# Kernel optimization log

Measured on AMD Instinct MI355X. Metric: run time of the kernel, lower is better.

The kernel has to match this reference:

```python
import jax, jax.numpy as jnp
import numpy as np

LN_EPS = 1e-5

def _layernorm(x, gamma, beta):
    mu = jnp.mean(x, axis=-1, keepdims=True)
    var = jnp.var(x, axis=-1, keepdims=True)
    return (x - mu) * jax.lax.rsqrt(var + LN_EPS) * gamma + beta

def setup_inputs() -> dict:
    key = jax.random.key(0)
    ks = jax.random.split(key, 4)
    B, s, d, L = 8, 192, 512, 8
    h = 2048  # embed_dim * 2
    return {
        "lags": jax.random.normal(ks[0], (B, s, d, L), dtype=jnp.float32),
        "gamma1": jnp.ones((d,), jnp.float32),
        "beta1": jnp.zeros((d,), jnp.float32),
        "W1": jax.random.normal(ks[1], (d, h), jnp.float32) * (1.0 / np.sqrt(d)),
        "b1": jnp.zeros((h,), jnp.float32),
        "W2": jax.random.normal(ks[2], (h, d), jnp.float32) * (1.0 / np.sqrt(h)),
        "b2": jnp.zeros((d,), jnp.float32),
        "gamma3": jnp.ones((d,), jnp.float32),
        "beta3": jnp.zeros((d,), jnp.float32),
    }

def reference(lags, gamma1, beta1, W1, b1, W2, b2, gamma3, beta3):
    B, s, d, L = lags.shape
    # (B, s, d, L) -> (B, s, L, d) -> (B, S=s*L, d)
    x = jnp.transpose(lags, (0, 1, 3, 2)).reshape(B, s * L, d)
    scale = 1.0 / jnp.sqrt(jnp.asarray(d, x.dtype))
    # single-head, unprojected attention: scores = X X^T / sqrt(d)
    scores = jnp.einsum('bqd,bkd->bqk', x, x) * scale  # [B, S, S]
    attn = jax.nn.softmax(scores, axis=-1)
    attn_out = jnp.einsum('bqk,bkd->bqd', attn, x)
    q = _layernorm(x + attn_out, gamma1, beta1)
    ff = jnp.dot(jax.nn.gelu(jnp.dot(q, W1) + b1, approximate=False), W2) + b2
    out = _layernorm(q + ff, gamma3, beta3)
    # (B, S, d) -> (B, s, L, d) -> (B, s, d, L)
    return jnp.transpose(out.reshape(B, s, L, d), (0, 1, 3, 2))
```

## Files before the change

kernel.cpp:

```cpp
#include <hip/hip_runtime.h>
#include <hip/hip_bf16.h>
#include <math.h>

#define B_ 8
#define S_ 192
#define D_ 512
#define L_ 8
#define SQ 1536
#define H_ 2048
#define NROW (B_*SQ)
#define SCALE_QK 0.04419417382415922f

typedef unsigned short ushort_t;
typedef unsigned int uint_t;
typedef __attribute__((ext_vector_type(8))) short bf16x8;
typedef __attribute__((ext_vector_type(4))) float f32x4;

__device__ __forceinline__ float bfu2f(ushort_t u) { return __uint_as_float((unsigned)u << 16); }
__device__ __forceinline__ ushort_t f2bfu(float f) {
  __hip_bfloat16 h = __float2bfloat16(f);
  return *reinterpret_cast<ushort_t*>(&h);
}

__device__ __forceinline__ float gelu_fast(float x) {
  float z = fabsf(x) * 0.70710678118654752f;
  float t = __builtin_amdgcn_rcpf(fmaf(0.3275911f, z, 1.0f));
  float p = fmaf(1.061405429f, t, -1.453152027f);
  p = fmaf(p, t, 1.421413741f);
  p = fmaf(p, t, -0.284496736f);
  p = fmaf(p, t, 0.254829592f);
  p = p * t;
  float e = __expf(-z * z);
  float erfz = fmaf(-p, e, 1.0f);
  float s = (x >= 0.0f) ? erfz : -erfz;
  return 0.5f * x * (1.0f + s);
}

__device__ __forceinline__ void gl_lds16(const ushort_t* g, ushort_t* l) {
  __builtin_amdgcn_global_load_lds(
      (const __attribute__((address_space(1))) unsigned int*)g,
      (__attribute__((address_space(3))) unsigned int*)l, 16, 0, 0);
}

__global__ __launch_bounds__(256) void k_build_x_f(const float* __restrict__ lags,
                                                   float* __restrict__ x,
                                                   ushort_t* __restrict__ x_bf) {
  __shared__ float tile[512][9];
  const int tid = threadIdx.x;
  const float* in = lags + (size_t)blockIdx.x * 4096;
  #pragma unroll
  for (int it = 0; it < 4; ++it) {
    int f = (tid + it * 256) * 4;
    float4 v = *reinterpret_cast<const float4*>(in + f);
    int k = f >> 3, l0 = f & 7;
    tile[k][l0] = v.x; tile[k][l0 + 1] = v.y; tile[k][l0 + 2] = v.z; tile[k][l0 + 3] = v.w;
  }
  __syncthreads();
  const int l = tid >> 5, kbase = tid & 31;
  const size_t r = (size_t)blockIdx.x * 8 + l;
  #pragma unroll
  for (int j = 0; j < 16; ++j) {
    int k = kbase + 32 * j;
    float v = tile[k][l];
    x[r * D_ + k] = v;
    x_bf[r * D_ + k] = f2bfu(v);
  }
}

__global__ __launch_bounds__(256) void k_xt(const ushort_t* __restrict__ x_bf,
                                            ushort_t* __restrict__ xT) {
  __shared__ ushort_t tile[64][65];
  int t0 = blockIdx.x * 64, d0 = blockIdx.y * 64;
  const ushort_t* X = x_bf + (size_t)blockIdx.z * SQ * D_;
  ushort_t* XT = xT + (size_t)blockIdx.z * SQ * D_;
  for (int i = threadIdx.x; i < 4096; i += 256) {
    int tt = i >> 6, dd = i & 63;
    tile[dd][tt] = X[(size_t)(t0 + tt) * D_ + d0 + dd];
  }
  __syncthreads();
  for (int i = threadIdx.x; i < 4096; i += 256) {
    int dd = i >> 6, tt = i & 63;
    XT[(size_t)(d0 + dd) * SQ + t0 + tt] = tile[dd][tt];
  }
}

__global__ __launch_bounds__(256) void k_wt(const float* __restrict__ W,
                                            ushort_t* __restrict__ Wt,
                                            int K, int N) {
  __shared__ ushort_t tile[64][65];
  int n0 = blockIdx.x * 64, k0 = blockIdx.y * 64;
  for (int i = threadIdx.x; i < 4096; i += 256) {
    int kk = i >> 6, nn = i & 63;
    tile[nn][kk] = f2bfu(W[(size_t)(k0 + kk) * N + n0 + nn]);
  }
  __syncthreads();
  for (int i = threadIdx.x; i < 4096; i += 256) {
    int nn = i >> 6, kk = i & 63;
    Wt[(size_t)(n0 + nn) * K + k0 + kk] = tile[nn][kk];
  }
}

template<int MODE>
__global__ __launch_bounds__(256) void k_gemm(const ushort_t* __restrict__ A,
                                              const ushort_t* __restrict__ Bt,
                                              const float* __restrict__ bias,
                                              void* __restrict__ Cout,
                                              int M, int K, int N,
                                              size_t sAz, size_t sBz, size_t sCz,
                                              float scale) {
  A  += (size_t)blockIdx.z * sAz;
  Bt += (size_t)blockIdx.z * sBz;
  __shared__ ushort_t As[128 * 64];
  __shared__ ushort_t Bs[128 * 64];
  const int tid = threadIdx.x;
  const int m0 = blockIdx.y * 128, n0 = blockIdx.x * 128;
  const int w = tid >> 6, lane = tid & 63;
  const int wr = w >> 1, wc = w & 1;
  const int l15 = lane & 15, quad = lane >> 4;
  const int lrow8 = lane >> 3;
  const int cg = ((lane & 7) ^ lrow8) * 8;
  const int xsw = l15 & 7;
  ushort_t* lA = &As[(w * 32) * 64];
  ushort_t* lB = &Bs[(w * 32) * 64];

  f32x4 acc[4][4];
  if (MODE <= 1) {
    #pragma unroll
    for (int nj = 0; nj < 4; ++nj) {
      float bv = bias[n0 + wc * 64 + nj * 16 + l15];
      #pragma unroll
      for (int mi = 0; mi < 4; ++mi) acc[mi][nj] = (f32x4){bv, bv, bv, bv};
    }
  } else {
    #pragma unroll
    for (int nj = 0; nj < 4; ++nj)
      #pragma unroll
      for (int mi = 0; mi < 4; ++mi) acc[mi][nj] = (f32x4){0.f, 0.f, 0.f, 0.f};
  }

  for (int k0 = 0; k0 < K; k0 += 64) {
    const ushort_t* gA = A  + (size_t)(m0 + w * 32 + lrow8) * K + k0 + cg;
    const ushort_t* gB = Bt + (size_t)(n0 + w * 32 + lrow8) * K + k0 + cg;
    __syncthreads();
    #pragma unroll
    for (int j = 0; j < 4; ++j) {
      gl_lds16(gA + (size_t)(j * 8) * K, lA + j * 8 * 64);
      gl_lds16(gB + (size_t)(j * 8) * K, lB + j * 8 * 64);
    }
    __syncthreads();
    #pragma unroll
    for (int kk = 0; kk < 2; ++kk) {
      const int csel = ((kk * 4 + quad) ^ xsw) * 8;
      bf16x8 af[4], bfv[4];
      #pragma unroll
      for (int mi = 0; mi < 4; ++mi)
        af[mi] = *reinterpret_cast<const bf16x8*>(&As[(wr * 64 + mi * 16 + l15) * 64 + csel]);
      #pragma unroll
      for (int nj = 0; nj < 4; ++nj)
        bfv[nj] = *reinterpret_cast<const bf16x8*>(&Bs[(wc * 64 + nj * 16 + l15) * 64 + csel]);
      #pragma unroll
      for (int mi = 0; mi < 4; ++mi)
        #pragma unroll
        for (int nj = 0; nj < 4; ++nj)
          acc[mi][nj] = __builtin_amdgcn_mfma_f32_16x16x32_bf16(af[mi], bfv[nj], acc[mi][nj], 0, 0, 0);
    }
  }

  ushort_t* Cb = (ushort_t*)Cout + (size_t)blockIdx.z * sCz;
  float*    Cf = (float*)Cout    + (size_t)blockIdx.z * sCz;
  #pragma unroll
  for (int mi = 0; mi < 4; ++mi)
    #pragma unroll
    for (int nj = 0; nj < 4; ++nj) {
      int gc = n0 + wc * 64 + nj * 16 + l15;
      #pragma unroll
      for (int r = 0; r < 4; ++r) {
        int gr = m0 + wr * 64 + mi * 16 + quad * 4 + r;
        float v = acc[mi][nj][r];
        if (MODE == 0) {
          Cb[(size_t)gr * N + gc] = f2bfu(gelu_fast(v));
        } else if (MODE == 1) {
          Cf[(size_t)gr * N + gc] = v;
        } else if (MODE == 2) {
          Cb[(size_t)gr * N + gc] = f2bfu(v * scale);
        } else {
          Cf[(size_t)gr * N + gc] = v;
        }
      }
    }
}

__global__ __launch_bounds__(256) void k_softmax_bf(ushort_t* __restrict__ sc) {
  uint_t* row = (uint_t*)(sc + (size_t)blockIdx.z * SQ * SQ + (size_t)blockIdx.x * SQ);
  int tid = threadIdx.x;
  __shared__ float red[8];
  float v[6];
  float m = -1e30f;
  #pragma unroll
  for (int k = 0; k < 3; ++k) {
    uint_t u = row[tid + k * 256];
    v[2*k]   = __uint_as_float(u << 16);
    v[2*k+1] = __uint_as_float(u & 0xffff0000u);
    m = fmaxf(m, fmaxf(v[2*k], v[2*k+1]));
  }
  #pragma unroll
  for (int o = 32; o > 0; o >>= 1) m = fmaxf(m, __shfl_down(m, o));
  if ((tid & 63) == 0) red[tid >> 6] = m;
  __syncthreads();
  m = fmaxf(fmaxf(red[0], red[1]), fmaxf(red[2], red[3]));
  __syncthreads();
  float ssum = 0.f;
  #pragma unroll
  for (int k = 0; k < 6; ++k) { v[k] = expf(v[k] - m); ssum += v[k]; }
  #pragma unroll
  for (int o = 32; o > 0; o >>= 1) ssum += __shfl_down(ssum, o);
  if ((tid & 63) == 0) red[4 + (tid >> 6)] = ssum;
  __syncthreads();
  float inv = 1.0f / (red[4] + red[5] + red[6] + red[7]);
  #pragma unroll
  for (int k = 0; k < 3; ++k) {
    uint_t lo = f2bfu(v[2*k] * inv);
    uint_t hi = f2bfu(v[2*k+1] * inv);
    row[tid + k * 256] = (hi << 16) | lo;
  }
}

__global__ __launch_bounds__(256) void k_ln1b(const float* __restrict__ x,
                                              const float* __restrict__ attn,
                                              const float* __restrict__ g,
                                              const float* __restrict__ be,
                                              ushort_t* __restrict__ qbf) {
  size_t base = (size_t)blockIdx.x * D_;
  int tid = threadIdx.x;
  __shared__ float rl[8];
  float v0 = x[base + tid] + attn[base + tid];
  float v1 = x[base + tid + 256] + attn[base + tid + 256];
  float s = v0 + v1, sq = v0 * v0 + v1 * v1;
  #pragma unroll
  for (int o = 32; o > 0; o >>= 1) { s += __shfl_down(s, o); sq += __shfl_down(sq, o); }
  int lane = tid & 63, wid = tid >> 6;
  if (lane == 0) { rl[wid] = s; rl[4 + wid] = sq; }
  __syncthreads();
  s = rl[0] + rl[1] + rl[2] + rl[3];
  sq = rl[4] + rl[5] + rl[6] + rl[7];
  float mean = s * (1.0f / 512.0f);
  float var = sq * (1.0f / 512.0f) - mean * mean;
  float rstd = rsqrtf(var + 1e-5f);
  qbf[base + tid]       = f2bfu((v0 - mean) * rstd * g[tid] + be[tid]);
  qbf[base + tid + 256] = f2bfu((v1 - mean) * rstd * g[tid + 256] + be[tid + 256]);
}

__global__ __launch_bounds__(256) void k_ln3_f(const float* __restrict__ y,
                                               const ushort_t* __restrict__ qbf,
                                               const float* __restrict__ g3,
                                               const float* __restrict__ be3,
                                               float* __restrict__ out) {
  __shared__ float ynorm[8][512];
  const int tid = threadIdx.x;
  const int w = tid >> 6, lane = tid & 63;
  #pragma unroll
  for (int rr = 0; rr < 2; ++rr) {
    int l = 2 * w + rr;
    size_t t = (size_t)blockIdx.x * 8 + l;
    float v[8];
    float s = 0.f, sq = 0.f;
    #pragma unroll
    for (int j = 0; j < 8; ++j) {
      int k = lane + 64 * j;
      v[j] = y[t * D_ + k] + bfu2f(qbf[t * D_ + k]);
      s += v[j]; sq += v[j] * v[j];
    }
    #pragma unroll
    for (int o = 32; o > 0; o >>= 1) { s += __shfl_down(s, o); sq += __shfl_down(sq, o); }
    s = __shfl(s, 0); sq = __shfl(sq, 0);
    float mean = s * (1.0f / 512.0f);
    float var = sq * (1.0f / 512.0f) - mean * mean;
    float rstd = rsqrtf(var + 1e-5f);
    #pragma unroll
    for (int j = 0; j < 8; ++j) {
      int k = lane + 64 * j;
      ynorm[l][k] = (v[j] - mean) * rstd * g3[k] + be3[k];
    }
  }
  __syncthreads();
  float* ob = out + (size_t)blockIdx.x * 4096;
  #pragma unroll
  for (int kk = 0; kk < 2; ++kk) {
    int k = tid * 2 + kk;
    float4 lo = make_float4(ynorm[0][k], ynorm[1][k], ynorm[2][k], ynorm[3][k]);
    float4 hi = make_float4(ynorm[4][k], ynorm[5][k], ynorm[6][k], ynorm[7][k]);
    *reinterpret_cast<float4*>(ob + (size_t)k * 8)     = lo;
    *reinterpret_cast<float4*>(ob + (size_t)k * 8 + 4) = hi;
  }
}

#define TS 64
#define KT 16
__global__ __launch_bounds__(256) void k_build_x_s(const float* __restrict__ lags,
                                                   float* __restrict__ x, int b_base) {
  int idx = blockIdx.x * 256 + threadIdx.x;
  int k = idx & (D_ - 1);
  int r = idx >> 9;
  int b = b_base + r / SQ;
  int t = r - (r / SQ) * SQ;
  int si = t >> 3, l = t & 7;
  size_t src = (((size_t)(b * S_ + si) * D_ + k) << 3) + l;
  x[idx] = lags[src];
}

__global__ __launch_bounds__(256) void k_scores(const float* __restrict__ x,
                                                float* __restrict__ sc, int b_base) {
  const float* A = x;
  float* C = sc;
  __shared__ float As[TS][KT + 1];
  __shared__ float Bs[TS][KT + 1];
  int tx = threadIdx.x & 15, ty = threadIdx.x >> 4;
  int j0 = blockIdx.x * TS, i0 = blockIdx.y * TS;
  float acc[4][4] = {};
  int lk = threadIdx.x & 15, lr = threadIdx.x >> 4;
  for (int k0 = 0; k0 < D_; k0 += KT) {
    #pragma unroll
    for (int it = 0; it < 4; ++it) {
      As[lr + 16 * it][lk] = A[(size_t)(i0 + lr + 16 * it) * D_ + k0 + lk];
      Bs[lr + 16 * it][lk] = A[(size_t)(j0 + lr + 16 * it) * D_ + k0 + lk];
    }
    __syncthreads();
    #pragma unroll
    for (int kk = 0; kk < KT; ++kk) {
      float a[4], bb[4];
      #pragma unroll
      for (int r = 0; r < 4; ++r) a[r] = As[ty * 4 + r][kk];
      #pragma unroll
      for (int c = 0; c < 4; ++c) bb[c] = Bs[tx * 4 + c][kk];
      #pragma unroll
      for (int r = 0; r < 4; ++r)
        #pragma unroll
        for (int c = 0; c < 4; ++c) acc[r][c] = fmaf(a[r], bb[c], acc[r][c]);
    }
    __syncthreads();
  }
  #pragma unroll
  for (int r = 0; r < 4; ++r) {
    float4 v = make_float4(acc[r][0]*SCALE_QK, acc[r][1]*SCALE_QK,
                           acc[r][2]*SCALE_QK, acc[r][3]*SCALE_QK);
    *reinterpret_cast<float4*>(&C[(size_t)(i0 + ty*4 + r) * SQ + j0 + tx*4]) = v;
  }
}

__global__ __launch_bounds__(256) void k_softmax(float* __restrict__ sc) {
  float* row = sc + (size_t)blockIdx.x * SQ;
  int tid = threadIdx.x;
  __shared__ float red[8];
  float m = -1e30f;
  for (int j = tid; j < SQ; j += 256) m = fmaxf(m, row[j]);
  #pragma unroll
  for (int o = 32; o > 0; o >>= 1) m = fmaxf(m, __shfl_down(m, o));
  if ((tid & 63) == 0) red[tid >> 6] = m;
  __syncthreads();
  m = fmaxf(fmaxf(red[0], red[1]), fmaxf(red[2], red[3]));
  __syncthreads();
  float ssum = 0.f;
  for (int j = tid; j < SQ; j += 256) { float e = expf(row[j] - m); row[j] = e; ssum += e; }
  #pragma unroll
  for (int o = 32; o > 0; o >>= 1) ssum += __shfl_down(ssum, o);
  if ((tid & 63) == 0) red[4 + (tid >> 6)] = ssum;
  __syncthreads();
  float inv = 1.0f / (red[4] + red[5] + red[6] + red[7]);
  for (int j = tid; j < SQ; j += 256) row[j] *= inv;
}

__global__ __launch_bounds__(256) void k_attn(const float* __restrict__ x,
                                              const float* __restrict__ sc,
                                              float* __restrict__ attn) {
  const float* X = x;
  const float* P = sc;
  float* O = attn;
  __shared__ float Ps[TS][KT + 1];
  __shared__ float Xs[KT][TS];
  int tx = threadIdx.x & 15, ty = threadIdx.x >> 4;
  int j0 = blockIdx.x * TS, i0 = blockIdx.y * TS;
  float acc[4][4] = {};
  int lk = threadIdx.x & 15, lr = threadIdx.x >> 4;
  int lc = threadIdx.x & 63, lrow = threadIdx.x >> 6;
  for (int k0 = 0; k0 < SQ; k0 += KT) {
    #pragma unroll
    for (int it = 0; it < 4; ++it)
      Ps[lr + 16 * it][lk] = P[(size_t)(i0 + lr + 16 * it) * SQ + k0 + lk];
    #pragma unroll
    for (int it = 0; it < 4; ++it)
      Xs[lrow + 4 * it][lc] = X[(size_t)(k0 + lrow + 4 * it) * D_ + j0 + lc];
    __syncthreads();
    #pragma unroll
    for (int kk = 0; kk < KT; ++kk) {
      float a[4], bb[4];
      #pragma unroll
      for (int r = 0; r < 4; ++r) a[r] = Ps[ty * 4 + r][kk];
      #pragma unroll
      for (int c = 0; c < 4; ++c) bb[c] = Xs[kk][tx * 4 + c];
      #pragma unroll
      for (int r = 0; r < 4; ++r)
        #pragma unroll
        for (int c = 0; c < 4; ++c) acc[r][c] = fmaf(a[r], bb[c], acc[r][c]);
    }
    __syncthreads();
  }
  #pragma unroll
  for (int r = 0; r < 4; ++r) {
    float4 v = make_float4(acc[r][0], acc[r][1], acc[r][2], acc[r][3]);
    *reinterpret_cast<float4*>(&O[(size_t)(i0 + ty*4 + r) * D_ + j0 + tx*4]) = v;
  }
}

__global__ __launch_bounds__(256) void k_ln1(const float* __restrict__ x,
                                             const float* __restrict__ attn,
                                             const float* __restrict__ g,
                                             const float* __restrict__ be,
                                             float* __restrict__ qout) {
  size_t base = (size_t)blockIdx.x * D_;
  int tid = threadIdx.x;
  __shared__ float rl[8];
  float v0 = x[base + tid] + attn[base + tid];
  float v1 = x[base + tid + 256] + attn[base + tid + 256];
  float s = v0 + v1, sq = v0 * v0 + v1 * v1;
  #pragma unroll
  for (int o = 32; o > 0; o >>= 1) { s += __shfl_down(s, o); sq += __shfl_down(sq, o); }
  int lane = tid & 63, wid = tid >> 6;
  if (lane == 0) { rl[wid] = s; rl[4 + wid] = sq; }
  __syncthreads();
  s = rl[0] + rl[1] + rl[2] + rl[3];
  sq = rl[4] + rl[5] + rl[6] + rl[7];
  float mean = s * (1.0f / 512.0f);
  float var = sq * (1.0f / 512.0f) - mean * mean;
  float rstd = rsqrtf(var + 1e-5f);
  qout[base + tid]       = (v0 - mean) * rstd * g[tid] + be[tid];
  qout[base + tid + 256] = (v1 - mean) * rstd * g[tid + 256] + be[tid + 256];
}

__global__ __launch_bounds__(256, 2) void k_ffn(
    const float* __restrict__ q,
    const float* __restrict__ W1, const float* __restrict__ b1,
    const float* __restrict__ W2, const float* __restrict__ b2,
    const float* __restrict__ g3, const float* __restrict__ be3,
    float* __restrict__ out, int row_base)
{
  __shared__ float qs[8][D_];
  __shared__ float mid[8][H_];
  const int tid = threadIdx.x;
  const int row0 = blockIdx.x * 8;
  for (int idx = tid; idx < 8 * D_; idx += 256)
    qs[idx >> 9][idx & (D_ - 1)] = q[(size_t)row0 * D_ + idx];
  __syncthreads();
  float acc[8][8];
  {
    float4 bA = *reinterpret_cast<const float4*>(b1 + (tid << 3));
    float4 bB = *reinterpret_cast<const float4*>(b1 + (tid << 3) + 4);
    float bv[8] = {bA.x, bA.y, bA.z, bA.w, bB.x, bB.y, bB.z, bB.w};
    #pragma unroll
    for (int jj = 0; jj < 8; ++jj)
      #pragma unroll
      for (int r = 0; r < 8; ++r) acc[jj][r] = bv[jj];
  }
  for (int k4 = 0; k4 < D_ / 4; ++k4) {
    float4 qv[8];
    #pragma unroll
    for (int r = 0; r < 8; ++r)
      qv[r] = *reinterpret_cast<const float4*>(&qs[r][k4 << 2]);
    #pragma unroll
    for (int kk = 0; kk < 4; ++kk) {
      const int k = (k4 << 2) + kk;
      float4 wA = *reinterpret_cast<const float4*>(W1 + (size_t)k * H_ + (tid << 3));
      float4 wB = *reinterpret_cast<const float4*>(W1 + (size_t)k * H_ + (tid << 3) + 4);
      float wv[8] = {wA.x, wA.y, wA.z, wA.w, wB.x, wB.y, wB.z, wB.w};
      #pragma unroll
      for (int r = 0; r < 8; ++r) {
        float qk = (kk == 0) ? qv[r].x : (kk == 1) ? qv[r].y : (kk == 2) ? qv[r].z : qv[r].w;
        #pragma unroll
        for (int jj = 0; jj < 8; ++jj) acc[jj][r] = fmaf(qk, wv[jj], acc[jj][r]);
      }
    }
  }
  #pragma unroll
  for (int jj = 0; jj < 8; ++jj)
    #pragma unroll
    for (int r = 0; r < 8; ++r) {
      float v = acc[jj][r];
      mid[r][(tid << 3) + jj] = 0.5f * v * (1.0f + erff(v * 0.70710678118654752f));
    }
  __syncthreads();
  float acc2[8][2];
  {
    float b20 = b2[tid << 1], b21 = b2[(tid << 1) + 1];
    #pragma unroll
    for (int r = 0; r < 8; ++r) { acc2[r][0] = b20; acc2[r][1] = b21; }
  }
  for (int j4 = 0; j4 < H_ / 4; ++j4) {
    float4 mv[8];
    #pragma unroll
    for (int r = 0; r < 8; ++r)
      mv[r] = *reinterpret_cast<const float4*>(&mid[r][j4 << 2]);
    #pragma unroll
    for (int kk = 0; kk < 4; ++kk) {
      const int j = (j4 << 2) + kk;
      float2 wv = *reinterpret_cast<const float2*>(W2 + (size_t)j * D_ + (tid << 1));
      #pragma unroll
      for (int r = 0; r < 8; ++r) {
        float m = (kk == 0) ? mv[r].x : (kk == 1) ? mv[r].y : (kk == 2) ? mv[r].z : mv[r].w;
        acc2[r][0] = fmaf(m, wv.x, acc2[r][0]);
        acc2[r][1] = fmaf(m, wv.y, acc2[r][1]);
      }
    }
  }
  __syncthreads();
  float* ys = &mid[0][0];
  #pragma unroll
  for (int r = 0; r < 8; ++r) {
    ys[r * D_ + (tid << 1)]     = qs[r][(tid << 1)]     + acc2[r][0];
    ys[r * D_ + (tid << 1) + 1] = qs[r][(tid << 1) + 1] + acc2[r][1];
  }
  __syncthreads();
  float g3a = g3[tid],  g3b = g3[tid + 256];
  float be3a = be3[tid], be3b = be3[tid + 256];
  float* rl = &qs[0][0];
  for (int r = 0; r < 8; ++r) {
    float v0 = ys[r * D_ + tid], v1 = ys[r * D_ + tid + 256];
    float s = v0 + v1, sq = v0 * v0 + v1 * v1;
    #pragma unroll
    for (int o = 32; o > 0; o >>= 1) { s += __shfl_down(s, o); sq += __shfl_down(sq, o); }
    int lane = tid & 63, wid = tid >> 6;
    if (lane == 0) { rl[wid] = s; rl[4 + wid] = sq; }
    __syncthreads();
    s = rl[0] + rl[1] + rl[2] + rl[3];
    sq = rl[4] + rl[5] + rl[6] + rl[7];
    __syncthreads();
    float mean = s * (1.0f / 512.0f);
    float var = sq * (1.0f / 512.0f) - mean * mean;
    float rstd = rsqrtf(var + 1e-5f);
    int t = row_base + row0 + r;
    int b = t / SQ, tt = t - b * SQ;
    int si = tt >> 3, l = tt & 7;
    size_t ob = (((size_t)(b * S_ + si) * D_) << 3) + l;
    out[ob + ((size_t)tid << 3)]         = (v0 - mean) * rstd * g3a + be3a;
    out[ob + ((size_t)(tid + 256) << 3)] = (v1 - mean) * rstd * g3b + be3b;
  }
}

extern "C" void kernel_launch(void* const* d_in, const int* in_sizes, int n_in,
                              void* d_out, int out_size, void* d_ws, size_t ws_size,
                              hipStream_t stream) {
  const float* lags   = (const float*)d_in[0];
  const float* gamma1 = (const float*)d_in[1];
  const float* beta1  = (const float*)d_in[2];
  const float* W1     = (const float*)d_in[3];
  const float* b1     = (const float*)d_in[4];
  const float* W2     = (const float*)d_in[5];
  const float* b2     = (const float*)d_in[6];
  const float* g3     = (const float*)d_in[7];
  const float* be3    = (const float*)d_in[8];
  float* out = (float*)d_out;

  float* ws = (float*)d_ws;
  const size_t NX  = (size_t)B_ * SQ * D_;
  const size_t NXB = (size_t)SQ * D_;
  const size_t NS  = (size_t)SQ * SQ;

  const size_t need_full = (3 * NX + 8 * NS) * sizeof(float);

  if (ws_size >= need_full) {
    float* x        = ws;
    float* attn     = x + NX;
    ushort_t* q_bf  = (ushort_t*)(attn + NX);
    ushort_t* w1t   = q_bf + NX;
    ushort_t* w2t   = w1t + (size_t)H_ * D_;
    ushort_t* region = w2t + (size_t)H_ * D_;
    ushort_t* sc_bf = region;
    ushort_t* x_bf  = region + 8 * NS;
    ushort_t* xT_bf = x_bf + NX;
    ushort_t* mid_bf = region;

    k_build_x_f<<<dim3(B_ * S_), 256, 0, stream>>>(lags, x, x_bf);
    k_xt<<<dim3(SQ / 64, D_ / 64, B_), 256, 0, stream>>>(x_bf, xT_bf);
    k_wt<<<dim3(H_ / 64, D_ / 64), 256, 0, stream>>>(W1, w1t, D_, H_);
    k_wt<<<dim3(D_ / 64, H_ / 64), 256, 0, stream>>>(W2, w2t, H_, D_);
    k_gemm<2><<<dim3(SQ / 128, SQ / 128, B_), 256, 0, stream>>>(
        x_bf, x_bf, nullptr, sc_bf, SQ, D_, SQ, NXB, NXB, NS, SCALE_QK);
    k_softmax_bf<<<dim3(SQ, 1, B_), 256, 0, stream>>>(sc_bf);
    k_gemm<3><<<dim3(D_ / 128, SQ / 128, B_), 256, 0, stream>>>(
        sc_bf, xT_bf, nullptr, attn, SQ, SQ, D_, NS, NXB, NXB, 1.0f);
    k_ln1b<<<dim3(NROW), 256, 0, stream>>>(x, attn, gamma1, beta1, q_bf);
    k_gemm<0><<<dim3(H_ / 128, NROW / 128, 1), 256, 0, stream>>>(
        q_bf, w1t, b1, mid_bf, NROW, D_, H_, 0, 0, 0, 1.0f);
    k_gemm<1><<<dim3(D_ / 128, NROW / 128, 1), 256, 0, stream>>>(
        mid_bf, w2t, b2, attn, NROW, H_, D_, 0, 0, 0, 1.0f);
    k_ln3_f<<<dim3(B_ * S_), 256, 0, stream>>>(attn, q_bf, g3, be3, out);
  } else {
    float* xb   = ws;
    float* sc   = xb + NXB;
    float* atb  = sc + NS;
    float* qb   = atb + NXB;
    for (int b = 0; b < B_; ++b) {
      k_build_x_s<<<dim3((unsigned)(NXB / 256)), 256, 0, stream>>>(lags, xb, b);
      k_scores<<<dim3(SQ / TS, SQ / TS, 1), 256, 0, stream>>>(xb, sc, b);
      k_softmax<<<dim3(SQ, 1, 1), 256, 0, stream>>>(sc);
      k_attn<<<dim3(D_ / TS, SQ / TS, 1), 256, 0, stream>>>(xb, sc, atb);
      k_ln1<<<dim3(SQ), 256, 0, stream>>>(xb, atb, gamma1, beta1, qb);
      k_ffn<<<dim3(SQ / 8), 256, 0, stream>>>(qb, W1, b1, W2, b2, g3, be3, out, b * SQ);
    }
  }
}
```

Before: 306.1 us.

## Store bf16 GEMM operands in pre-swizzled 64-wide k-panel layout

Introduces a panel-major swizzled layout (k-blocks of 64, rows contiguous within a panel, XOR-swizzled 8-element groups) for every bf16 intermediate: x_bf, xT, transposed weights, scores/probabilities, gelu output and LN1 output. Producers write directly into this layout, so each GEMM k-tile becomes one contiguous 16 KB chunk that global_load_lds can fetch with fully linear addresses instead of strided row segments. This is meant to cut address arithmetic and improve coalescing and TLB behaviour on the tile loads. In exchange, producer kernels (softmax, layernorm, epilogues) now make scattered, less coalesced stores and carry extra index math, and every kernel touching these buffers has to agree on the layout.

```diff
diff --git a/kernel.cpp b/kernel.cpp
--- a/kernel.cpp
+++ b/kernel.cpp
@@ -20,6 +20,10 @@
 __device__ __forceinline__ ushort_t f2bfu(float f) {
   __hip_bfloat16 h = __float2bfloat16(f);
   return *reinterpret_cast<ushort_t*>(&h);
+}
+
+__device__ __forceinline__ size_t pidx(int row, int k, int R) {
+  return ((size_t)(k >> 6) * R + row) * 64 + ((((k >> 3) & 7) ^ (row & 7)) << 3) + (k & 7);
 }
 
 __device__ __forceinline__ float gelu_fast(float x) {
@@ -57,13 +61,15 @@
   }
   __syncthreads();
   const int l = tid >> 5, kbase = tid & 31;
-  const size_t r = (size_t)blockIdx.x * 8 + l;
+  const int r = blockIdx.x * 8 + l;
+  const int b = r / SQ, rloc = r - b * SQ;
+  ushort_t* xb = x_bf + (size_t)b * SQ * D_;
   #pragma unroll
   for (int j = 0; j < 16; ++j) {
     int k = kbase + 32 * j;
     float v = tile[k][l];
-    x[r * D_ + k] = v;
-    x_bf[r * D_ + k] = f2bfu(v);
+    x[(size_t)r * D_ + k] = v;
+    xb[pidx(rloc, k, SQ)] = f2bfu(v);
   }
 }
 
@@ -75,12 +81,12 @@
   ushort_t* XT = xT + (size_t)blockIdx.z * SQ * D_;
   for (int i = threadIdx.x; i < 4096; i += 256) {
     int tt = i >> 6, dd = i & 63;
-    tile[dd][tt] = X[(size_t)(t0 + tt) * D_ + d0 + dd];
+    tile[dd][tt] = X[pidx(t0 + tt, d0 + dd, SQ)];
   }
   __syncthreads();
   for (int i = threadIdx.x; i < 4096; i += 256) {
     int dd = i >> 6, tt = i & 63;
-    XT[(size_t)(d0 + dd) * SQ + t0 + tt] = tile[dd][tt];
+    XT[pidx(d0 + dd, t0 + tt, D_)] = tile[dd][tt];
   }
 }
 
@@ -96,7 +102,7 @@
   __syncthreads();
   for (int i = threadIdx.x; i < 4096; i += 256) {
     int nn = i >> 6, kk = i & 63;
-    Wt[(size_t)(n0 + nn) * K + k0 + kk] = tile[nn][kk];
+    Wt[pidx(n0 + nn, k0 + kk, N)] = tile[nn][kk];
   }
 }
 
@@ -117,8 +123,6 @@
   const int w = tid >> 6, lane = tid & 63;
   const int wr = w >> 1, wc = w & 1;
   const int l15 = lane & 15, quad = lane >> 4;
-  const int lrow8 = lane >> 3;
-  const int cg = ((lane & 7) ^ lrow8) * 8;
   const int xsw = l15 & 7;
   ushort_t* lA = &As[(w * 32) * 64];
   ushort_t* lB = &Bs[(w * 32) * 64];
@@ -138,14 +142,15 @@
       for (int mi = 0; mi < 4; ++mi) acc[mi][nj] = (f32x4){0.f, 0.f, 0.f, 0.f};
   }
 
-  for (int k0 = 0; k0 < K; k0 += 64) {
-    const ushort_t* gA = A  + (size_t)(m0 + w * 32 + lrow8) * K + k0 + cg;
-    const ushort_t* gB = Bt + (size_t)(n0 + w * 32 + lrow8) * K + k0 + cg;
+  const int NT = K >> 6;
+  for (int t = 0; t < NT; ++t) {
+    const ushort_t* gA = A  + ((size_t)t * M + m0 + w * 32) * 64 + lane * 8;
+    const ushort_t* gB = Bt + ((size_t)t * N + n0 + w * 32) * 64 + lane * 8;
     __syncthreads();
     #pragma unroll
     for (int j = 0; j < 4; ++j) {
-      gl_lds16(gA + (size_t)(j * 8) * K, lA + j * 8 * 64);
-      gl_lds16(gB + (size_t)(j * 8) * K, lB + j * 8 * 64);
+      gl_lds16(gA + j * 512, lA + j * 512);
+      gl_lds16(gB + j * 512, lB + j * 512);
     }
     __syncthreads();
     #pragma unroll
@@ -178,11 +183,11 @@
         int gr = m0 + wr * 64 + mi * 16 + quad * 4 + r;
         float v = acc[mi][nj][r];
         if (MODE == 0) {
-          Cb[(size_t)gr * N + gc] = f2bfu(gelu_fast(v));
+          Cb[pidx(gr, gc, M)] = f2bfu(gelu_fast(v));
         } else if (MODE == 1) {
           Cf[(size_t)gr * N + gc] = v;
         } else if (MODE == 2) {
-          Cb[(size_t)gr * N + gc] = f2bfu(v * scale);
+          Cb[pidx(gr, gc, M)] = f2bfu(v * scale);
         } else {
           Cf[(size_t)gr * N + gc] = v;
         }
@@ -191,17 +196,21 @@
 }
 
 __global__ __launch_bounds__(256) void k_softmax_bf(ushort_t* __restrict__ sc) {
-  uint_t* row = (uint_t*)(sc + (size_t)blockIdx.z * SQ * SQ + (size_t)blockIdx.x * SQ);
+  ushort_t* base = sc + (size_t)blockIdx.z * SQ * SQ;
+  const int r = blockIdx.x;
   int tid = threadIdx.x;
   __shared__ float red[8];
+  uint_t addr[3];
   float v[6];
   float m = -1e30f;
   #pragma unroll
-  for (int k = 0; k < 3; ++k) {
-    uint_t u = row[tid + k * 256];
-    v[2*k]   = __uint_as_float(u << 16);
-    v[2*k+1] = __uint_as_float(u & 0xffff0000u);
-    m = fmaxf(m, fmaxf(v[2*k], v[2*k+1]));
+  for (int j = 0; j < 3; ++j) {
+    int k2 = 2 * tid + 512 * j;
+    addr[j] = (uint_t)(pidx(r, k2, SQ) >> 1);
+    uint_t u = ((uint_t*)base)[addr[j]];
+    v[2*j]   = __uint_as_float(u << 16);
+    v[2*j+1] = __uint_as_float(u & 0xffff0000u);
+    m = fmaxf(m, fmaxf(v[2*j], v[2*j+1]));
   }
   #pragma unroll
   for (int o = 32; o > 0; o >>= 1) m = fmaxf(m, __shfl_down(m, o));
@@ -218,10 +227,10 @@
   __syncthreads();
   float inv = 1.0f / (red[4] + red[5] + red[6] + red[7]);
   #pragma unroll
-  for (int k = 0; k < 3; ++k) {
-    uint_t lo = f2bfu(v[2*k] * inv);
-    uint_t hi = f2bfu(v[2*k+1] * inv);
-    row[tid + k * 256] = (hi << 16) | lo;
+  for (int j = 0; j < 3; ++j) {
+    uint_t lo = f2bfu(v[2*j] * inv);
+    uint_t hi = f2bfu(v[2*j+1] * inv);
+    ((uint_t*)base)[addr[j]] = (hi << 16) | lo;
   }
 }
 
@@ -230,7 +239,8 @@
                                               const float* __restrict__ g,
                                               const float* __restrict__ be,
                                               ushort_t* __restrict__ qbf) {
-  size_t base = (size_t)blockIdx.x * D_;
+  const int row = blockIdx.x;
+  size_t base = (size_t)row * D_;
   int tid = threadIdx.x;
   __shared__ float rl[8];
   float v0 = x[base + tid] + attn[base + tid];
@@ -246,8 +256,8 @@
   float mean = s * (1.0f / 512.0f);
   float var = sq * (1.0f / 512.0f) - mean * mean;
   float rstd = rsqrtf(var + 1e-5f);
-  qbf[base + tid]       = f2bfu((v0 - mean) * rstd * g[tid] + be[tid]);
-  qbf[base + tid + 256] = f2bfu((v1 - mean) * rstd * g[tid + 256] + be[tid + 256]);
+  qbf[pidx(row, tid, NROW)]       = f2bfu((v0 - mean) * rstd * g[tid] + be[tid]);
+  qbf[pidx(row, tid + 256, NROW)] = f2bfu((v1 - mean) * rstd * g[tid + 256] + be[tid + 256]);
 }
 
 __global__ __launch_bounds__(256) void k_ln3_f(const float* __restrict__ y,
@@ -261,13 +271,13 @@
   #pragma unroll
   for (int rr = 0; rr < 2; ++rr) {
     int l = 2 * w + rr;
-    size_t t = (size_t)blockIdx.x * 8 + l;
+    int t = blockIdx.x * 8 + l;
     float v[8];
     float s = 0.f, sq = 0.f;
     #pragma unroll
     for (int j = 0; j < 8; ++j) {
       int k = lane + 64 * j;
-      v[j] = y[t * D_ + k] + bfu2f(qbf[t * D_ + k]);
+      v[j] = y[(size_t)t * D_ + k] + bfu2f(qbf[pidx(t, k, NROW)]);
       s += v[j]; sq += v[j] * v[j];
     }
     #pragma unroll
```

Result: slower. 315.7 us (+3.2%).
